# Kernel tuning notes

Measured on AMD Instinct MI355X. Metric: run time of the kernel, lower is better.

Reference implementation:

```python
import jax, jax.numpy as jnp
import numpy as np

# ---- module hyperparameters (from init_kwargs) ----
FREQ_RANGE = (100.0, 8000.0)
CHANNELS = 128
BW_FACTOR = 1.0
SAMPLE_RATE = 16000
ORDER = 4                    # gammatone order (4 cascaded one-pole sections)
ATT_HALF_BW_DB = -3.0        # pyfilterbank default attenuation at half bandwidth


def _hertz_to_erbscale(f):
    return 21.4 * np.log10(4.37e-3 * f + 1.0)


def _erbscale_to_hertz(e):
    return (10.0 ** (e / 21.4) - 1.0) / 4.37e-3


def _design_bank():
    """Replicates pyfilterbank.gammatone: frequencies_gammatone_bank + design_filter.
    normfreq=0 so the ERB offset term is zero."""
    sb = _hertz_to_erbscale(FREQ_RANGE[0])
    eb = _hertz_to_erbscale(FREQ_RANGE[1])
    density = (eb - sb) / (CHANNELS - 0.05)
    cf = _erbscale_to_hertz(np.arange(sb, eb, density))        # [C] center freqs (Hz)
    erb_aud = 24.7 * (4.37e-3 * cf + 1.0)                      # audiological ERB
    phi = np.pi * BW_FACTOR * erb_aud / SAMPLE_RATE
    alpha = 10.0 ** (0.1 * ATT_HALF_BW_DB / ORDER)
    p = (-2.0 + 2.0 * alpha * np.cos(phi)) / (1.0 - alpha)
    lam = -p / 2.0 - np.sqrt(p * p / 4.0 - 1.0)
    beta = 2.0 * np.pi * cf / SAMPLE_RATE
    coef = lam * np.exp(1j * beta)                             # complex pole [C]
    factor = 2.0 * (1.0 - np.abs(coef)) ** ORDER               # stage-1 gain [C]
    return coef, factor


def setup_inputs() -> dict:
    key = jax.random.key(0)
    inp = jax.random.normal(key, (8, 32000), dtype=jnp.float32)  # [B, T] waveforms
    coef, factor = _design_bank()
    return {
        "inp": inp,
        "coef_re": jnp.asarray(np.real(coef), dtype=jnp.float32),  # [C]
        "coef_im": jnp.asarray(np.imag(coef), dtype=jnp.float32),  # [C]
        "factor": jnp.asarray(factor, dtype=jnp.float32),          # [C]
    }


def reference(inp, coef_re, coef_im, factor):
    """Gammatone filterbank analysis: 4 cascaded complex one-pole IIR sections
    per band, applied to every (batch, band) pair in parallel; returns the real
    part, shaped [B, T, C] like the original module's np stacking/transpose."""
    coef = (coef_re + 1j * coef_im).astype(jnp.complex64)          # [C]
    B, T = inp.shape
    C = coef.shape[0]
    # time-major stage input: [T, B, C]; stage 1 applies the gain `factor`
    y = inp.T[:, :, None].astype(jnp.complex64) * factor.astype(jnp.complex64)
    s0 = jnp.zeros((B, C), dtype=jnp.complex64)

    def one_pole(x):
        # s[t] = coef * s[t-1] + x[t], zero initial state (lfilter zi=0)
        def step(s, xt):
            s = coef * s + xt
            return s, s
        _, out = jax.lax.scan(step, s0, x)
        return out

    for _ in range(ORDER):   # fixed small cascade, stages 2..4 have b0 = 1
        y = one_pole(y)
    return jnp.real(y).transpose(1, 0, 2).astype(jnp.float32)      # [B, T, C]
```

## Files before the change

kernel.cpp:

```cpp
#include <hip/hip_runtime.h>


#define B_N    8
#define T_LEN  32000
#define C_CH   128
#define L_CHK  500
#define NB     64
#define W_MAX  1024

#define STEP(XR) do {                                          \
    const float xr  = (XR) * f;                                \
    const float n1r = fmaf(cr, s1r, fmaf(-ci, s1i, xr));       \
    const float n1i = fmaf(cr, s1i, ci * s1r);                 \
    const float n2r = fmaf(cr, s2r, fmaf(-ci, s2i, n1r));      \
    const float n2i = fmaf(cr, s2i, fmaf(ci, s2r, n1i));       \
    const float n3r = fmaf(cr, s3r, fmaf(-ci, s3i, n2r));      \
    const float n3i = fmaf(cr, s3i, fmaf(ci, s3r, n2i));       \
    const float n4r = fmaf(cr, s4r, fmaf(-ci, s4i, n3r));      \
    const float n4i = fmaf(cr, s4i, fmaf(ci, s4r, n3i));       \
    s1r=n1r; s1i=n1i; s2r=n2r; s2i=n2i;                        \
    s3r=n3r; s3i=n3i; s4r=n4r; s4i=n4i;                        \
} while (0)

__global__ __launch_bounds__(64) void gt_trunc(
    const float* __restrict__ x, const float* __restrict__ cre,
    const float* __restrict__ cim, const float* __restrict__ fac,
    float* __restrict__ out)
{
    __shared__ __align__(16) float xs[L_CHK + W_MAX];
    const int g  = blockIdx.x;
    const int k  = blockIdx.y;
    const int b  = blockIdx.z;
    const int c  = g * 64 + threadIdx.x;
    const int t0 = k * L_CHK;

    const float cr0 = cre[g * 64], ci0 = cim[g * 64];
    const float negln = -0.5f * __logf(cr0 * cr0 + ci0 * ci0);
    int W = (int)ceilf(24.0f / negln) + 2;
    W = (W + 3) & ~3;
    if (W > W_MAX) W = W_MAX;
    int start = t0 - W;
    if (start < 0) start = 0;
    const int n  = t0 + L_CHK - start;
    const int nw = t0 - start;

    const float* xb = x + (size_t)b * T_LEN + start;
    for (int i = threadIdx.x; i < n; i += 64) xs[i] = xb[i];

    const float cr = cre[c], ci = cim[c], f = fac[c];
    __syncthreads();

    float s1r=0.f,s1i=0.f,s2r=0.f,s2i=0.f,s3r=0.f,s3i=0.f,s4r=0.f,s4i=0.f;

    for (int i = 0; i < nw; i += 4) {
        const float4 xq = *(const float4*)&xs[i];
        STEP(xq.x); STEP(xq.y); STEP(xq.z); STEP(xq.w);
    }

    float* op = out + ((size_t)b * T_LEN + t0) * C_CH + c;
    for (int i = 0; i < L_CHK; i += 4) {
        const float4 xq = *(const float4*)&xs[nw + i];
        STEP(xq.x); op[(size_t)(i + 0) * C_CH] = s4r;
        STEP(xq.y); op[(size_t)(i + 1) * C_CH] = s4r;
        STEP(xq.z); op[(size_t)(i + 2) * C_CH] = s4r;
        STEP(xq.w); op[(size_t)(i + 3) * C_CH] = s4r;
    }
}

extern "C" void kernel_launch(void* const* d_in, const int* in_sizes, int n_in,
                              void* d_out, int out_size, void* d_ws, size_t ws_size,
                              hipStream_t stream) {
    const float* x   = (const float*)d_in[0];
    const float* cre = (const float*)d_in[1];
    const float* cim = (const float*)d_in[2];
    const float* fac = (const float*)d_in[3];
    float* out = (float*)d_out;

    gt_trunc<<<dim3(2, NB, B_N), 64, 0, stream>>>(x, cre, cim, fac, out);
}
```

Baseline: 163.3 us.

## Pack complex IIR state into float2 vectors, shorten warmup window, defer gain

Measured after the change: 160.3 us. About the same (-1.9%).

```diff
diff --git a/kernel.cpp b/kernel.cpp
--- a/kernel.cpp
+++ b/kernel.cpp
@@ -1,5 +1,7 @@
 #include <hip/hip_runtime.h>
 
+
+typedef float f32x2 __attribute__((ext_vector_type(2)));
 
 #define B_N    8
 #define T_LEN  32000
@@ -8,18 +10,13 @@
 #define NB     64
 #define W_MAX  1024
 
-#define STEP(XR) do {                                          \
-    const float xr  = (XR) * f;                                \
-    const float n1r = fmaf(cr, s1r, fmaf(-ci, s1i, xr));       \
-    const float n1i = fmaf(cr, s1i, ci * s1r);                 \
-    const float n2r = fmaf(cr, s2r, fmaf(-ci, s2i, n1r));      \
-    const float n2i = fmaf(cr, s2i, fmaf(ci, s2r, n1i));       \
-    const float n3r = fmaf(cr, s3r, fmaf(-ci, s3i, n2r));      \
-    const float n3i = fmaf(cr, s3i, fmaf(ci, s3r, n2i));       \
-    const float n4r = fmaf(cr, s4r, fmaf(-ci, s4i, n3r));      \
-    const float n4i = fmaf(cr, s4i, fmaf(ci, s4r, n3i));       \
-    s1r=n1r; s1i=n1i; s2r=n2r; s2i=n2i;                        \
-    s3r=n3r; s3i=n3i; s4r=n4r; s4i=n4i;                        \
+#define CSTEP(XR) do {                              \
+    const f32x2 xin = {(XR), 0.f};                  \
+    f32x2 t;                                        \
+    t = crr * s1 + xin;  s1 = cni * s1.yx + t;      \
+    t = crr * s2 + s1;   s2 = cni * s2.yx + t;      \
+    t = crr * s3 + s2;   s3 = cni * s3.yx + t;      \
+    t = crr * s4 + s3;   s4 = cni * s4.yx + t;      \
 } while (0)
 
 __global__ __launch_bounds__(64) void gt_trunc(
@@ -27,7 +24,7 @@
     const float* __restrict__ cim, const float* __restrict__ fac,
     float* __restrict__ out)
 {
-    __shared__ __align__(16) float xs[L_CHK + W_MAX];
+    __shared__ __align__(16) float xs[L_CHK + W_MAX + 4];
     const int g  = blockIdx.x;
     const int k  = blockIdx.y;
     const int b  = blockIdx.z;
@@ -36,7 +33,7 @@
 
     const float cr0 = cre[g * 64], ci0 = cim[g * 64];
     const float negln = -0.5f * __logf(cr0 * cr0 + ci0 * ci0);
-    int W = (int)ceilf(24.0f / negln) + 2;
+    int W = (int)ceilf(18.0f / negln) + 2;
     W = (W + 3) & ~3;
     if (W > W_MAX) W = W_MAX;
     int start = t0 - W;
@@ -48,22 +45,27 @@
     for (int i = threadIdx.x; i < n; i += 64) xs[i] = xb[i];
 
     const float cr = cre[c], ci = cim[c], f = fac[c];
+    const f32x2 crr = {cr, cr};
+    const f32x2 cni = {-ci, ci};
     __syncthreads();
 
-    float s1r=0.f,s1i=0.f,s2r=0.f,s2i=0.f,s3r=0.f,s3i=0.f,s4r=0.f,s4i=0.f;
+    f32x2 s1 = {0.f, 0.f}, s2 = {0.f, 0.f}, s3 = {0.f, 0.f}, s4 = {0.f, 0.f};
 
+    float4 cur = *(const float4*)&xs[0];
     for (int i = 0; i < nw; i += 4) {
-        const float4 xq = *(const float4*)&xs[i];
-        STEP(xq.x); STEP(xq.y); STEP(xq.z); STEP(xq.w);
+        const float4 nxt = *(const float4*)&xs[i + 4];
+        CSTEP(cur.x); CSTEP(cur.y); CSTEP(cur.z); CSTEP(cur.w);
+        cur = nxt;
     }
 
     float* op = out + ((size_t)b * T_LEN + t0) * C_CH + c;
-    for (int i = 0; i < L_CHK; i += 4) {
-        const float4 xq = *(const float4*)&xs[nw + i];
-        STEP(xq.x); op[(size_t)(i + 0) * C_CH] = s4r;
-        STEP(xq.y); op[(size_t)(i + 1) * C_CH] = s4r;
-        STEP(xq.z); op[(size_t)(i + 2) * C_CH] = s4r;
-        STEP(xq.w); op[(size_t)(i + 3) * C_CH] = s4r;
+    for (int j = 0; j < L_CHK; j += 4) {
+        const float4 nxt = *(const float4*)&xs[nw + j + 4];
+        CSTEP(cur.x); op[(size_t)(j + 0) * C_CH] = s4.x * f;
+        CSTEP(cur.y); op[(size_t)(j + 1) * C_CH] = s4.x * f;
+        CSTEP(cur.z); op[(size_t)(j + 2) * C_CH] = s4.x * f;
+        CSTEP(cur.w); op[(size_t)(j + 3) * C_CH] = s4.x * f;
+        cur = nxt;
     }
 }
 
```
